# Kernel optimization log

Hardware: AMD Instinct MI355X
Metric: run time of the kernel (lower is better)

Reference implementation:

```python
import jax, jax.numpy as jnp
import numpy as np

IN_F, OUT_F = 4096, 11008
MAXQ = 15  # 2**4 - 1 for wbits=4


def setup_inputs() -> dict:
    key = jax.random.key(0)
    k1, k2, k3, k4, k5 = jax.random.split(key, 5)
    inp = jax.random.normal(k1, (4, 64, IN_F), dtype=jnp.float32)
    weight = jax.random.normal(k2, (OUT_F, IN_F), dtype=jnp.float32) * 0.02
    bias = jax.random.normal(k3, (OUT_F,), dtype=jnp.float32) * 0.02
    # per-channel asymmetric quant params (as Quantizer.find_params would produce)
    scale = jax.random.uniform(k4, (OUT_F, 1), dtype=jnp.float32) * 0.01 + 1e-4
    zero = jnp.round(jax.random.uniform(k5, (OUT_F, 1), dtype=jnp.float32) * MAXQ)
    return {"input": inp, "weight": weight, "bias": bias,
            "scale": scale, "zero": zero, "maxq": MAXQ}


def reference(input, weight, bias, scale, zero, maxq):
    # fake-quantize weight: q = clamp(round(w/scale) + zero, 0, maxq); w_dq = scale*(q - zero)
    q = jnp.clip(jnp.round(weight / scale) + zero, 0.0, float(maxq))
    w_dq = scale * (q - zero)                      # [out, in]
    # F.linear: input @ w_dq.T + bias
    out = jnp.einsum('bsi,oi->bso', input, w_dq) + bias
    return out
```

## Files before the change

### kernel.cpp

```cpp
#include <hip/hip_runtime.h>
#include <hip/hip_bf16.h>
#include <stdint.h>

#define K_TOT 4096
#define N_TOT 11008
#define M_TOT 256
#define BM 128
#define BN 64
#define WST 72

using bf16x8 = __attribute__((ext_vector_type(8))) short;
using f32x4  = __attribute__((ext_vector_type(4))) float;

__global__ void cvt_a_bf16(const float* __restrict__ in, uint32_t* __restrict__ out) {
    int i = blockIdx.x * blockDim.x + threadIdx.x;
    const float4 v = ((const float4*)in)[i];
    uint32_t a = __float_as_uint(v.x), b = __float_as_uint(v.y),
             c = __float_as_uint(v.z), d = __float_as_uint(v.w);
    a += 0x7FFFu + ((a >> 16) & 1u);
    b += 0x7FFFu + ((b >> 16) & 1u);
    c += 0x7FFFu + ((c >> 16) & 1u);
    d += 0x7FFFu + ((d >> 16) & 1u);
    uint2 o;
    o.x = (a >> 16) | (b & 0xFFFF0000u);
    o.y = (c >> 16) | (d & 0xFFFF0000u);
    ((uint2*)out)[i] = o;
}

__device__ __forceinline__ void dequant16(const float4 w[4], float rs, float zp, float sc,
                                          uint32_t o[8]) {
    float f[16];
#pragma unroll
    for (int j = 0; j < 4; ++j) {
        f[4 * j + 0] = w[j].x; f[4 * j + 1] = w[j].y;
        f[4 * j + 2] = w[j].z; f[4 * j + 3] = w[j].w;
    }
    uint32_t u[16];
#pragma unroll
    for (int i = 0; i < 16; ++i) {
        float q = rintf(f[i] * rs) + zp;
        q = fminf(fmaxf(q, 0.0f), 15.0f);
        float dq = (q - zp) * sc;
        uint32_t b = __float_as_uint(dq);
        u[i] = b + 0x7FFFu + ((b >> 16) & 1u);
    }
#pragma unroll
    for (int i = 0; i < 8; ++i)
        o[i] = (u[2 * i] >> 16) | (u[2 * i + 1] & 0xFFFF0000u);
}

__device__ __forceinline__ void compute_step(f32x4 acc[4][2], const uint16_t* const Ap[4],
                                             const uint16_t (*sw)[WST], int kt, int wn, int lane) {
    const int koff = kt * 64;
#pragma unroll
    for (int s = 0; s < 2; ++s) {
        bf16x8 a[4], b[2];
#pragma unroll
        for (int mi = 0; mi < 4; ++mi)
            a[mi] = *(const bf16x8*)(Ap[mi] + koff + s * 32);
#pragma unroll
        for (int ni = 0; ni < 2; ++ni)
            b[ni] = *(const bf16x8*)&sw[wn + ni * 16 + (lane & 15)][s * 32 + (lane >> 4) * 8];
#pragma unroll
        for (int mi = 0; mi < 4; ++mi)
#pragma unroll
            for (int ni = 0; ni < 2; ++ni)
                acc[mi][ni] = __builtin_amdgcn_mfma_f32_16x16x32_bf16(a[mi], b[ni], acc[mi][ni], 0, 0, 0);
    }
}

__global__ __launch_bounds__(256, 4)
void wql_gemm(const uint16_t* __restrict__ A,
              const float* __restrict__ W,
              const float* __restrict__ scale,
              const float* __restrict__ zero,
              float* __restrict__ P,
              int kloc) {
    __shared__ uint16_t sW[2][BN][WST];

    const int tid  = threadIdx.x;
    const int lane = tid & 63;
    const int wv   = tid >> 6;
    const int wm   = (wv & 1) * 64;
    const int wn   = (wv >> 1) * 32;
    const int m0   = blockIdx.x * BM;
    const int n0   = blockIdx.y * BN;
    const int k0   = blockIdx.z * kloc;
    const int nkt  = kloc / 64;

    const int nloc = tid >> 2;
    const int kseg = tid & 3;
    const int wrow = n0 + nloc;
    const float* Wp = W + (size_t)wrow * K_TOT + k0 + kseg * 16;
    const float sc = scale[wrow];
    const float zp = zero[wrow];
    const float rs = 1.0f / sc;
    uint16_t* sdst0 = &sW[0][nloc][kseg * 16];
    uint16_t* sdst1 = &sW[1][nloc][kseg * 16];

    const uint16_t* Ap[4];
#pragma unroll
    for (int mi = 0; mi < 4; ++mi)
        Ap[mi] = A + (size_t)(m0 + wm + mi * 16 + (lane & 15)) * K_TOT + k0 + (lane >> 4) * 8;

    f32x4 acc[4][2];
#pragma unroll
    for (int mi = 0; mi < 4; ++mi)
#pragma unroll
        for (int ni = 0; ni < 2; ++ni)
            acc[mi][ni] = (f32x4){0.f, 0.f, 0.f, 0.f};

    float4 bank0[4], bank1[4];

#pragma unroll
    for (int j = 0; j < 4; ++j) bank0[j] = ((const float4*)Wp)[j];
    {
        uint32_t o[8];
        dequant16(bank0, rs, zp, sc, o);
        ((uint4*)sdst0)[0] = make_uint4(o[0], o[1], o[2], o[3]);
        ((uint4*)sdst0)[1] = make_uint4(o[4], o[5], o[6], o[7]);
    }
#pragma unroll
    for (int j = 0; j < 4; ++j) bank1[j] = ((const float4*)(Wp + 64))[j];
    __syncthreads();

    for (int kt = 0; kt < nkt; kt += 2) {
        if (kt + 2 < nkt) {
            const float4* p = (const float4*)(Wp + (size_t)(kt + 2) * 64);
#pragma unroll
            for (int j = 0; j < 4; ++j) bank0[j] = p[j];
        }
        compute_step(acc, Ap, sW[0], kt, wn, lane);
        {
            uint32_t o[8];
            dequant16(bank1, rs, zp, sc, o);
            ((uint4*)sdst1)[0] = make_uint4(o[0], o[1], o[2], o[3]);
            ((uint4*)sdst1)[1] = make_uint4(o[4], o[5], o[6], o[7]);
        }
        __syncthreads();

        if (kt + 3 < nkt) {
            const float4* p = (const float4*)(Wp + (size_t)(kt + 3) * 64);
#pragma unroll
            for (int j = 0; j < 4; ++j) bank1[j] = p[j];
        }
        compute_step(acc, Ap, sW[1], kt + 1, wn, lane);
        if (kt + 2 < nkt) {
            uint32_t o[8];
            dequant16(bank0, rs, zp, sc, o);
            ((uint4*)sdst0)[0] = make_uint4(o[0], o[1], o[2], o[3]);
            ((uint4*)sdst0)[1] = make_uint4(o[4], o[5], o[6], o[7]);
        }
        __syncthreads();
    }

    float* Pb = P + (size_t)blockIdx.z * M_TOT * N_TOT;
    const int colbase = n0 + wn + (lane & 15);
    const int rbase = m0 + wm + ((lane >> 4) << 2);
#pragma unroll
    for (int mi = 0; mi < 4; ++mi) {
#pragma unroll
        for (int ni = 0; ni < 2; ++ni) {
            const int col = colbase + ni * 16;
#pragma unroll
            for (int r = 0; r < 4; ++r) {
                const int row = rbase + mi * 16 + r;
                Pb[(size_t)row * N_TOT + col] = acc[mi][ni][r];
            }
        }
    }
}

__global__ void reduce_bias(const float* __restrict__ P, const float* __restrict__ bias,
                            float* __restrict__ out, int ks) {
    const int i4 = blockIdx.x * blockDim.x + threadIdx.x;
    const size_t tot4 = (size_t)M_TOT * N_TOT / 4;
    const int col = (int)(((size_t)i4 * 4) % N_TOT);
    float4 acc = ((const float4*)P)[i4];
    for (int s = 1; s < ks; ++s) {
        const float4 v = ((const float4*)P)[(size_t)s * tot4 + i4];
        acc.x += v.x; acc.y += v.y; acc.z += v.z; acc.w += v.w;
    }
    const float4 b = *(const float4*)(bias + col);
    acc.x += b.x; acc.y += b.y; acc.z += b.z; acc.w += b.w;
    ((float4*)out)[i4] = acc;
}

extern "C" void kernel_launch(void* const* d_in, const int* in_sizes, int n_in,
                              void* d_out, int out_size, void* d_ws, size_t ws_size,
                              hipStream_t stream) {
    const float* inp    = (const float*)d_in[0];
    const float* weight = (const float*)d_in[1];
    const float* bias   = (const float*)d_in[2];
    const float* scale  = (const float*)d_in[3];
    const float* zero   = (const float*)d_in[4];

    const size_t A_BYTES = (size_t)M_TOT * K_TOT * 2;
    const size_t SLICE   = (size_t)M_TOT * N_TOT * 4;

    uint32_t* Abf = (uint32_t*)d_ws;
    float* partial;
    int KS;
    if (ws_size >= A_BYTES + 4 * SLICE) { KS = 4; partial = (float*)((char*)d_ws + A_BYTES); }
    else if (ws_size >= A_BYTES + 2 * SLICE) { KS = 2; partial = (float*)((char*)d_ws + A_BYTES); }
    else { KS = 1; partial = (float*)d_out; }

    cvt_a_bf16<<<dim3((M_TOT * K_TOT / 4) / 256), dim3(256), 0, stream>>>(inp, Abf);

    dim3 grid(M_TOT / BM, N_TOT / BN, KS);
    wql_gemm<<<grid, dim3(256), 0, stream>>>((const uint16_t*)Abf, weight, scale, zero,
                                             partial, K_TOT / KS);

    reduce_bias<<<dim3((M_TOT * N_TOT / 4) / 256), dim3(256), 0, stream>>>(
        partial, bias, (float*)d_out, KS);
}
```

Baseline: 365.4 us.

## Deepen weight prefetch pipeline, simplify dequant math, use nontemporal loads/stores

Widens the weight register prefetch from two banks to four, so global loads run three k-steps ahead, and unrolls the main loop by four. Dequant folds the zero point into the clamp bounds and uses med3 and perm builtins, cutting ALU ops per weight. Weight loads and partial-sum traffic use nontemporal loads and stores, and the barrier is replaced by an explicit lgkmcnt wait plus s_barrier. Occupancy hint drops from 4 to 3 waves per EU to make room for the extra prefetch registers. The folded dequant computes rint(w/s) clamped to [-z, 15-z] times s, which is algebraically the same as the reference.

```diff
diff --git a/kernel.cpp b/kernel.cpp
--- a/kernel.cpp
+++ b/kernel.cpp
@@ -1,5 +1,4 @@
 #include <hip/hip_runtime.h>
-#include <hip/hip_bf16.h>
 #include <stdint.h>
 
 #define K_TOT 4096
@@ -11,6 +10,12 @@
 
 using bf16x8 = __attribute__((ext_vector_type(8))) short;
 using f32x4  = __attribute__((ext_vector_type(4))) float;
+
+#define BAR() do {                                          \
+    asm volatile("s_waitcnt lgkmcnt(0)" ::: "memory");      \
+    __builtin_amdgcn_s_barrier();                           \
+    asm volatile("" ::: "memory");                          \
+} while (0)
 
 __global__ void cvt_a_bf16(const float* __restrict__ in, uint32_t* __restrict__ out) {
     int i = blockIdx.x * blockDim.x + threadIdx.x;
@@ -27,49 +32,41 @@
     ((uint2*)out)[i] = o;
 }
 
-__device__ __forceinline__ void dequant16(const float4 w[4], float rs, float zp, float sc,
-                                          uint32_t o[8]) {
-    float f[16];
+__device__ __forceinline__ uint32_t pack_hi16(uint32_t u0, uint32_t u1) {
+#if __has_builtin(__builtin_amdgcn_perm)
+    return __builtin_amdgcn_perm(u1, u0, 0x07060302u);
+#else
+    return (u0 >> 16) | (u1 & 0xFFFF0000u);
+#endif
+}
+
+__device__ __forceinline__ float clamp3(float q, float lo, float hi) {
+#if __has_builtin(__builtin_amdgcn_fmed3f)
+    return __builtin_amdgcn_fmed3f(q, lo, hi);
+#else
+    return fminf(fmaxf(q, lo), hi);
+#endif
+}
+
+__device__ __forceinline__ void dequant16(const f32x4* w, float rs, float lo, float hi,
+                                          float sc, uint32_t o[8]) {
+    uint32_t u[16];
 #pragma unroll
     for (int j = 0; j < 4; ++j) {
-        f[4 * j + 0] = w[j].x; f[4 * j + 1] = w[j].y;
-        f[4 * j + 2] = w[j].z; f[4 * j + 3] = w[j].w;
-    }
-    uint32_t u[16];
-#pragma unroll
-    for (int i = 0; i < 16; ++i) {
-        float q = rintf(f[i] * rs) + zp;
-        q = fminf(fmaxf(q, 0.0f), 15.0f);
-        float dq = (q - zp) * sc;
-        uint32_t b = __float_as_uint(dq);
-        u[i] = b + 0x7FFFu + ((b >> 16) & 1u);
-    }
-#pragma unroll
-    for (int i = 0; i < 8; ++i)
-        o[i] = (u[2 * i] >> 16) | (u[2 * i + 1] & 0xFFFF0000u);
-}
-
-__device__ __forceinline__ void compute_step(f32x4 acc[4][2], const uint16_t* const Ap[4],
-                                             const uint16_t (*sw)[WST], int kt, int wn, int lane) {
-    const int koff = kt * 64;
-#pragma unroll
-    for (int s = 0; s < 2; ++s) {
-        bf16x8 a[4], b[2];
-#pragma unroll
-        for (int mi = 0; mi < 4; ++mi)
-            a[mi] = *(const bf16x8*)(Ap[mi] + koff + s * 32);
-#pragma unroll
-        for (int ni = 0; ni < 2; ++ni)
-            b[ni] = *(const bf16x8*)&sw[wn + ni * 16 + (lane & 15)][s * 32 + (lane >> 4) * 8];
-#pragma unroll
-        for (int mi = 0; mi < 4; ++mi)
-#pragma unroll
-            for (int ni = 0; ni < 2; ++ni)
-                acc[mi][ni] = __builtin_amdgcn_mfma_f32_16x16x32_bf16(a[mi], b[ni], acc[mi][ni], 0, 0, 0);
-    }
-}
-
-__global__ __launch_bounds__(256, 4)
+#pragma unroll
+        for (int e = 0; e < 4; ++e) {
+            float q  = rintf(w[j][e] * rs);
+            q        = clamp3(q, lo, hi);
+            float dq = q * sc;
+            uint32_t b = __float_as_uint(dq);
+            u[4 * j + e] = b + 0x7FFFu + ((b >> 16) & 1u);
+        }
+    }
+#pragma unroll
+    for (int i = 0; i < 8; ++i) o[i] = pack_hi16(u[2 * i], u[2 * i + 1]);
+}
+
+__global__ __launch_bounds__(256, 3)
 void wql_gemm(const uint16_t* __restrict__ A,
               const float* __restrict__ W,
               const float* __restrict__ scale,
@@ -86,7 +83,7 @@
     const int m0   = blockIdx.x * BM;
     const int n0   = blockIdx.y * BN;
     const int k0   = blockIdx.z * kloc;
-    const int nkt  = kloc / 64;
+    const int nkt  = kloc >> 6;
 
     const int nloc = tid >> 2;
     const int kseg = tid & 3;
@@ -95,8 +92,7 @@
     const float sc = scale[wrow];
     const float zp = zero[wrow];
     const float rs = 1.0f / sc;
-    uint16_t* sdst0 = &sW[0][nloc][kseg * 16];
-    uint16_t* sdst1 = &sW[1][nloc][kseg * 16];
+    const float lo = -zp, hi = 15.0f - zp;
 
     const uint16_t* Ap[4];
 #pragma unroll
@@ -110,48 +106,66 @@
         for (int ni = 0; ni < 2; ++ni)
             acc[mi][ni] = (f32x4){0.f, 0.f, 0.f, 0.f};
 
-    float4 bank0[4], bank1[4];
-
-#pragma unroll
-    for (int j = 0; j < 4; ++j) bank0[j] = ((const float4*)Wp)[j];
+    f32x4 bank[4][4];
+
+#pragma unroll
+    for (int s = 0; s < 3; ++s) {
+        const f32x4* p = (const f32x4*)(Wp + (size_t)s * 64);
+#pragma unroll
+        for (int j = 0; j < 4; ++j) bank[s][j] = __builtin_nontemporal_load(p + j);
+    }
     {
         uint32_t o[8];
-        dequant16(bank0, rs, zp, sc, o);
-        ((uint4*)sdst0)[0] = make_uint4(o[0], o[1], o[2], o[3]);
-        ((uint4*)sdst0)[1] = make_uint4(o[4], o[5], o[6], o[7]);
-    }
-#pragma unroll
-    for (int j = 0; j < 4; ++j) bank1[j] = ((const float4*)(Wp + 64))[j];
-    __syncthreads();
-
-    for (int kt = 0; kt < nkt; kt += 2) {
-        if (kt + 2 < nkt) {
-            const float4* p = (const float4*)(Wp + (size_t)(kt + 2) * 64);
-#pragma unroll
-            for (int j = 0; j < 4; ++j) bank0[j] = p[j];
+        dequant16(bank[0], rs, lo, hi, sc, o);
+        uint16_t* d = &sW[0][nloc][kseg * 16];
+        ((uint4*)d)[0] = make_uint4(o[0], o[1], o[2], o[3]);
+        ((uint4*)d)[1] = make_uint4(o[4], o[5], o[6], o[7]);
+    }
+    BAR();
+
+    for (int st = 0; st < nkt; st += 4) {
+#pragma unroll
+        for (int u = 0; u < 4; ++u) {
+            const int step = st + u;
+
+            if (step + 3 < nkt) {
+                const f32x4* p = (const f32x4*)(Wp + (size_t)(step + 3) * 64);
+#pragma unroll
+                for (int j = 0; j < 4; ++j)
+                    bank[(u + 3) & 3][j] = __builtin_nontemporal_load(p + j);
+            }
+
+            {
+                const int koff = step * 64;
+#pragma unroll
+                for (int s = 0; s < 2; ++s) {
+                    bf16x8 a[4], b[2];
+#pragma unroll
+                    for (int mi = 0; mi < 4; ++mi)
+                        a[mi] = *(const bf16x8*)(Ap[mi] + koff + s * 32);
+#pragma unroll
+                    for (int ni = 0; ni < 2; ++ni)
+                        b[ni] = *(const bf16x8*)&sW[u & 1][wn + ni * 16 + (lane & 15)]
+                                                  [s * 32 + (lane >> 4) * 8];
+#pragma unroll
+                    for (int mi = 0; mi < 4; ++mi)
+#pragma unroll
+                        for (int ni = 0; ni < 2; ++ni)
+                            acc[mi][ni] = __builtin_amdgcn_mfma_f32_16x16x32_bf16(
+                                a[mi], b[ni], acc[mi][ni], 0, 0, 0);
+                }
+            }
+
+            if (step + 1 < nkt) {
+                uint32_t o[8];
+                dequant16(bank[(u + 1) & 3], rs, lo, hi, sc, o);
+                uint16_t* d = &sW[(u + 1) & 1][nloc][kseg * 16];
+                ((uint4*)d)[0] = make_uint4(o[0], o[1], o[2], o[3]);
+                ((uint4*)d)[1] = make_uint4(o[4], o[5], o[6], o[7]);
+            }
+
+            BAR();
         }
-        compute_step(acc, Ap, sW[0], kt, wn, lane);
-        {
-            uint32_t o[8];
-            dequant16(bank1, rs, zp, sc, o);
-            ((uint4*)sdst1)[0] = make_uint4(o[0], o[1], o[2], o[3]);
-            ((uint4*)sdst1)[1] = make_uint4(o[4], o[5], o[6], o[7]);
-        }
-        __syncthreads();
-
-        if (kt + 3 < nkt) {
-            const float4* p = (const float4*)(Wp + (size_t)(kt + 3) * 64);
-#pragma unroll
-            for (int j = 0; j < 4; ++j) bank1[j] = p[j];
-        }
-        compute_step(acc, Ap, sW[1], kt + 1, wn, lane);
-        if (kt + 2 < nkt) {
-            uint32_t o[8];
-            dequant16(bank0, rs, zp, sc, o);
-            ((uint4*)sdst0)[0] = make_uint4(o[0], o[1], o[2], o[3]);
-            ((uint4*)sdst0)[1] = make_uint4(o[4], o[5], o[6], o[7]);
-        }
-        __syncthreads();
     }
 
     float* Pb = P + (size_t)blockIdx.z * M_TOT * N_TOT;
@@ -165,7 +179,7 @@
 #pragma unroll
             for (int r = 0; r < 4; ++r) {
                 const int row = rbase + mi * 16 + r;
-                Pb[(size_t)row * N_TOT + col] = acc[mi][ni][r];
+                __builtin_nontemporal_store(acc[mi][ni][r], &Pb[(size_t)row * N_TOT + col]);
             }
         }
     }
@@ -176,14 +190,14 @@
     const int i4 = blockIdx.x * blockDim.x + threadIdx.x;
     const size_t tot4 = (size_t)M_TOT * N_TOT / 4;
     const int col = (int)(((size_t)i4 * 4) % N_TOT);
-    float4 acc = ((const float4*)P)[i4];
+    f32x4 acc = __builtin_nontemporal_load((const f32x4*)P + i4);
     for (int s = 1; s < ks; ++s) {
-        const float4 v = ((const float4*)P)[(size_t)s * tot4 + i4];
-        acc.x += v.x; acc.y += v.y; acc.z += v.z; acc.w += v.w;
+        const f32x4 v = __builtin_nontemporal_load((const f32x4*)P + (size_t)s * tot4 + i4);
+        acc += v;
     }
     const float4 b = *(const float4*)(bias + col);
-    acc.x += b.x; acc.y += b.y; acc.z += b.z; acc.w += b.w;
-    ((float4*)out)[i4] = acc;
+    acc[0] += b.x; acc[1] += b.y; acc[2] += b.z; acc[3] += b.w;
+    *((f32x4*)out + i4) = acc;
 }
 
 extern "C" void kernel_launch(void* const* d_in, const int* in_sizes, int n_in,
```

New measurement: 407.7 us. +11.6%, slower.
